# Kernel optimization log

Measured on AMD Instinct MI355X. Metric: run time of the kernel, lower is better.

Reference implementation:

```python
import jax, jax.numpy as jnp
import numpy as np

D = 128      # dim_emb
FF = 512     # dim_ff
H = 8        # nb_heads
HD = D // H
NLE = 2      # encoder layers (action and state)
NLD = 2      # decoder layers
NS = 1       # num_state_encoder
TANH_CLIP = 10.0
BIG = jnp.float32(1e9)


def layer_norm(h, g, b):
    mu = jnp.mean(h, -1, keepdims=True)
    v = jnp.var(h, -1, keepdims=True)
    return g * (h - mu) * jax.lax.rsqrt(v + 1e-5) + b


def mha_self(h, Wq, Wk, Wv, Wo, bq, bk, bv, bo):
    B, S, _ = h.shape
    q = (h @ Wq + bq).reshape(B, S, H, HD)
    k = (h @ Wk + bk).reshape(B, S, H, HD)
    v = (h @ Wv + bv).reshape(B, S, H, HD)
    a = jax.nn.softmax(jnp.einsum('bqhd,bkhd->bhqk', q, k) / np.float32(np.sqrt(HD)), axis=-1)
    return jnp.einsum('bhqk,bkhd->bqhd', a, v).reshape(B, S, D) @ Wo + bo


def encode(tok, Wemb, bemb, aW, aB, W1, b1, W2, b2, ln):
    # tok: [B, S, 2] raw coordinates -> [B, S, D]
    h = tok @ Wemb + bemb
    for l in range(NLE):
        h = layer_norm(h + mha_self(h, *aW[l], *aB[l]), ln[l, 0, 0], ln[l, 0, 1])
        ffo = jax.nn.relu(h @ W1[l] + b1[l]) @ W2[l] + b2[l]
        h = layer_norm(h + ffo, ln[l, 1, 0], ln[l, 1, 1])
    return h


def _forward(x, start_idx, action_k, state_k,
             a_emb_W, a_emb_b, a_attn_W, a_attn_b, a_ff_W1, a_ff_b1, a_ff_W2, a_ff_b2, a_ln,
             s_emb_W, s_emb_b, s_attn_W, s_attn_b, s_ff_W1, s_ff_b1, s_ff_W2, s_ff_b2, s_ln,
             WK, bK, WV, bV, Wq_mlp, bq_mlp, d_Wq, d_bq, d_Wo, d_bo):
    B, N, _ = x.shape
    bar = jnp.arange(B)
    first = x[bar, start_idx]                                   # [B,2]
    mask0 = jnp.ones((B, N), bool).at[bar, start_idx].set(False)  # True = unvisited
    ka, ks = action_k, state_k

    def step(carry, _):
        mask, last_idx, logp = carry
        last = x[bar, last_idx]                                  # [B,2]
        # knn over unvisited nodes (visited nodes pushed to distance BIG)
        d2 = jnp.sum((x - last[:, None, :]) ** 2, -1)
        d2 = jnp.where(mask, d2, BIG)
        _, knn_idx = jax.lax.top_k(-d2, ks)                      # [B,ks] nearest-first global node ids
        aidx = knn_idx[:, :ka]                                   # [B,ka]
        valid = mask[bar[:, None], aidx]                         # unvisited -> valid action
        # action encoder: k_action neighbors + last visited node
        tok_a = jnp.concatenate([x[bar[:, None], aidx], last[:, None, :]], 1)       # [B,ka+1,2]
        emb_a = encode(tok_a, a_emb_W, a_emb_b, a_attn_W, a_attn_b, a_ff_W1, a_ff_b1, a_ff_W2, a_ff_b2, a_ln)
        emb_q = emb_a[:, ka]
        emb_o = emb_a[:, :ka]
        # state encoder: k_state neighbors + last + first visited node
        tok_s = jnp.concatenate([x[bar[:, None], knn_idx], last[:, None, :], first[:, None, :]], 1)  # [B,ks+2,2]
        emb_s = encode(tok_s, s_emb_W, s_emb_b, s_attn_W, s_attn_b, s_ff_W1, s_ff_b1, s_ff_W2, s_ff_b2, s_ln)
        emb_q = jnp.concatenate([emb_q, emb_s[:, ks], emb_s[:, ks + 1]], -1)        # [B,(2*NS+1)*D]
        emb_o = jnp.concatenate([emb_o, emb_s[:, :ka]], -1)                          # [B,ka,(NS+1)*D]
        # decoder: per-layer K/V slices, masked cross-attention, final tanh-clipped pointer
        h = emb_q @ Wq_mlp + bq_mlp                              # [B,D]
        K = (emb_o @ WK + bK).reshape(B, ka, NLD, D)
        V = (emb_o @ WV + bV).reshape(B, ka, NLD, D)
        for l in range(NLD - 1):
            q = (h @ d_Wq[l] + d_bq[l]).reshape(B, H, HD)
            kk = K[:, :, l].reshape(B, ka, H, HD)
            vv = V[:, :, l].reshape(B, ka, H, HD)
            sc = jnp.einsum('bhd,bkhd->bhk', q, kk) / np.float32(np.sqrt(HD))
            sc = jnp.where(valid[:, None, :], sc, -BIG)
            o = jnp.einsum('bhk,bkhd->bhd', jax.nn.softmax(sc, -1), vv).reshape(B, D) @ d_Wo[l] + d_bo[l]
            h = h + o
        q = h @ d_Wq[NLD - 1] + d_bq[NLD - 1]
        logits = TANH_CLIP * jnp.tanh(jnp.einsum('bd,bkd->bk', q, K[:, :, NLD - 1]) / np.float32(np.sqrt(D)))
        logits = jnp.where(valid, logits, -BIG)
        prob = jax.nn.softmax(logits, -1)
        idx = jnp.argmax(prob, 1)                                # deterministic choice
        nxt = aidx[bar, idx]
        logp = logp + jnp.log(prob[bar, idx])
        mask = mask.at[bar, nxt].set(False)
        return (mask, nxt, logp), nxt

    (_, _, logp), ys = jax.lax.scan(step, (mask0, start_idx, jnp.zeros(B, jnp.float32)), None, length=N - 1)
    tours = jnp.concatenate([start_idx[:, None], ys.T], 1)       # [B,N]
    return tours, logp


def setup_inputs() -> dict:
    key = jax.random.key(0)
    ks = jax.random.split(key, 16)
    def Nrm(k, shape, fan):
        return jax.random.normal(k, shape, jnp.float32) / np.float32(np.sqrt(fan))
    B, Nn = 64, 50
    inp = {}
    inp['x'] = jax.random.uniform(ks[0], (B, Nn, 2), jnp.float32)
    inp['start_idx'] = jax.random.randint(ks[1], (B,), 0, Nn)
    inp['action_k'] = 15
    inp['state_k'] = 35
    inp['a_emb_W'] = Nrm(ks[2], (2, D), 2); inp['a_emb_b'] = jnp.zeros((D,))
    inp['a_attn_W'] = Nrm(ks[3], (NLE, 4, D, D), D); inp['a_attn_b'] = jnp.zeros((NLE, 4, D))
    inp['a_ff_W1'] = Nrm(ks[4], (NLE, D, FF), D); inp['a_ff_b1'] = jnp.zeros((NLE, FF))
    inp['a_ff_W2'] = Nrm(ks[5], (NLE, FF, D), FF); inp['a_ff_b2'] = jnp.zeros((NLE, D))
    inp['a_ln'] = jnp.stack([jnp.ones((NLE, 2, D)), jnp.zeros((NLE, 2, D))], 2)
    inp['s_emb_W'] = Nrm(ks[6], (2, D), 2); inp['s_emb_b'] = jnp.zeros((D,))
    inp['s_attn_W'] = Nrm(ks[7], (NLE, 4, D, D), D); inp['s_attn_b'] = jnp.zeros((NLE, 4, D))
    inp['s_ff_W1'] = Nrm(ks[8], (NLE, D, FF), D); inp['s_ff_b1'] = jnp.zeros((NLE, FF))
    inp['s_ff_W2'] = Nrm(ks[9], (NLE, FF, D), FF); inp['s_ff_b2'] = jnp.zeros((NLE, D))
    inp['s_ln'] = jnp.stack([jnp.ones((NLE, 2, D)), jnp.zeros((NLE, 2, D))], 2)
    inp['WK'] = Nrm(ks[10], ((NS + 1) * D, NLD * D), (NS + 1) * D); inp['bK'] = jnp.zeros((NLD * D,))
    inp['WV'] = Nrm(ks[11], ((NS + 1) * D, NLD * D), (NS + 1) * D); inp['bV'] = jnp.zeros((NLD * D,))
    inp['Wq_mlp'] = Nrm(ks[12], ((2 * NS + 1) * D, D), (2 * NS + 1) * D); inp['bq_mlp'] = jnp.zeros((D,))
    inp['d_Wq'] = Nrm(ks[13], (NLD, D, D), D); inp['d_bq'] = jnp.zeros((NLD, D))
    inp['d_Wo'] = Nrm(ks[14], (NLD, D, D), D); inp['d_bo'] = jnp.zeros((NLD, D))
    return inp


def reference(x, start_idx, action_k, state_k,
              a_emb_W, a_emb_b, a_attn_W, a_attn_b, a_ff_W1, a_ff_b1, a_ff_W2, a_ff_b2, a_ln,
              s_emb_W, s_emb_b, s_attn_W, s_attn_b, s_ff_W1, s_ff_b1, s_ff_W2, s_ff_b2, s_ln,
              WK, bK, WV, bV, Wq_mlp, bq_mlp, d_Wq, d_bq, d_Wo, d_bo):
    return _forward(x, start_idx, action_k, state_k,
                    a_emb_W, a_emb_b, a_attn_W, a_attn_b, a_ff_W1, a_ff_b1, a_ff_W2, a_ff_b2, a_ln,
                    s_emb_W, s_emb_b, s_attn_W, s_attn_b, s_ff_W1, s_ff_b1, s_ff_W2, s_ff_b2, s_ln,
                    WK, bK, WV, bV, Wq_mlp, bq_mlp, d_Wq, d_bq, d_Wo, d_bo)
```

## Files before the change

kernel.cpp:

```cpp
#include <hip/hip_runtime.h>
#include <hip/hip_bf16.h>

namespace {

constexpr int NB  = 64;
constexpr int NN  = 50;
constexpr int DM  = 128;
constexpr int FFDIM = 512;
constexpr int NHD = 8;
constexpr int HDM = 16;
constexpr int KA  = 15;
constexpr int KS  = 35;
constexpr int TA  = 16;
constexpr int TS  = 37;
constexpr int NT  = 512;
constexpr float BIGF = 1000000000.0f;

constexpr int OFF_H    = 0;
constexpr int OFF_EMBA = TS * DM;
constexpr int OFF_SCR  = OFF_EMBA + TA * DM;
constexpr int SCR_FLOATS = 3 * TS * DM + NHD * TS * TS;
constexpr int SMEM_FLOATS = OFF_SCR + SCR_FLOATS;
constexpr int SMEM_BYTES  = SMEM_FLOATS * 4;

struct Params {
  const float* x; const int* start;
  const float* a_emb_W; const float* a_emb_b;
  const float* a_attn_W; const float* a_attn_b;
  const float* a_ff_W1; const float* a_ff_b1;
  const float* a_ff_W2; const float* a_ff_b2;
  const float* a_ln;
  const float* s_emb_W; const float* s_emb_b;
  const float* s_attn_W; const float* s_attn_b;
  const float* s_ff_W1; const float* s_ff_b1;
  const float* s_ff_W2; const float* s_ff_b2;
  const float* s_ln;
  const float* WK; const float* bK;
  const float* WV; const float* bV;
  const float* Wq_mlp; const float* bq_mlp;
  const float* d_Wq; const float* d_bq;
  const float* d_Wo; const float* d_bo;
  float* out;
};

template<int R>
__device__ inline void matmul_rt(const float* __restrict__ in, int lda,
                                 const float* __restrict__ W, int ldw,
                                 const float* __restrict__ bias,
                                 float* __restrict__ out, int ldo,
                                 int T, int K, int C, bool relu, int tid)
{
  const int c4 = C >> 2;
  const int cw = tid & (c4 - 1);
  const int g  = tid / c4;
  const int ng = NT / c4;
  const int c  = cw << 2;
  const float4 bv = *(const float4*)(bias + c);
#define FMA16_(aa, i) \
  acc[i].x = fmaf((aa).x, w0.x, acc[i].x); acc[i].y = fmaf((aa).x, w0.y, acc[i].y); \
  acc[i].z = fmaf((aa).x, w0.z, acc[i].z); acc[i].w = fmaf((aa).x, w0.w, acc[i].w); \
  acc[i].x = fmaf((aa).y, w1.x, acc[i].x); acc[i].y = fmaf((aa).y, w1.y, acc[i].y); \
  acc[i].z = fmaf((aa).y, w1.z, acc[i].z); acc[i].w = fmaf((aa).y, w1.w, acc[i].w); \
  acc[i].x = fmaf((aa).z, w2.x, acc[i].x); acc[i].y = fmaf((aa).z, w2.y, acc[i].y); \
  acc[i].z = fmaf((aa).z, w2.z, acc[i].z); acc[i].w = fmaf((aa).z, w2.w, acc[i].w); \
  acc[i].x = fmaf((aa).w, w3.x, acc[i].x); acc[i].y = fmaf((aa).w, w3.y, acc[i].y); \
  acc[i].z = fmaf((aa).w, w3.z, acc[i].z); acc[i].w = fmaf((aa).w, w3.w, acc[i].w);
  for (int rb = g * R; rb < T; rb += ng * R) {
    float4 acc[R];
#pragma unroll
    for (int i = 0; i < R; ++i) acc[i] = bv;
    const float* __restrict__ wp = W + c;
    const float* __restrict__ ip = in + rb * lda;
#pragma unroll 2
    for (int kk = 0; kk < K; kk += 4) {
      float4 w0 = *(const float4*)(wp + (size_t)(kk    ) * ldw);
      float4 w1 = *(const float4*)(wp + (size_t)(kk + 1) * ldw);
      float4 w2 = *(const float4*)(wp + (size_t)(kk + 2) * ldw);
      float4 w3 = *(const float4*)(wp + (size_t)(kk + 3) * ldw);
#pragma unroll
      for (int i = 0; i < R; ++i) {
        float4 a = *(const float4*)(ip + i * lda + kk);
        FMA16_(a, i);
      }
    }
#pragma unroll
    for (int i = 0; i < R; ++i) {
      if (rb + i < T) {
        float4 r2 = acc[i];
        if (relu) {
          r2.x = fmaxf(r2.x, 0.f); r2.y = fmaxf(r2.y, 0.f);
          r2.z = fmaxf(r2.z, 0.f); r2.w = fmaxf(r2.w, 0.f);
        }
        *(float4*)(out + (rb + i) * ldo + c) = r2;
      }
    }
  }
#undef FMA16_
}

__device__ inline void matvec128(const float* __restrict__ in, const float* __restrict__ W,
                                 const float* __restrict__ bias, float* __restrict__ out,
                                 int K, float* __restrict__ red, int tid)
{
  const int c = tid & 127;
  const int s = tid >> 7;
  const int ks = K >> 2;
  const int k0 = s * ks;
  float acc = 0.f;
#pragma unroll 8
  for (int k = k0; k < k0 + ks; ++k) acc = fmaf(in[k], W[(size_t)k * 128 + c], acc);
  red[tid] = acc;
  __syncthreads();
  if (tid < 128) out[c] = bias[c] + ((red[c] + red[128 + c]) + (red[256 + c] + red[384 + c]));
  __syncthreads();
}

__device__ inline void layernorm_add(float* __restrict__ h, const float* __restrict__ add,
                                     const float* __restrict__ g, const float* __restrict__ bta,
                                     int T, int tid)
{
  const int lane = tid & 63;
  const int wv = tid >> 6;
  for (int r = wv; r < T; r += NT / 64) {
    float v0 = h[r * DM + lane]      + add[r * DM + lane];
    float v1 = h[r * DM + lane + 64] + add[r * DM + lane + 64];
    float sum = v0 + v1;
    for (int off = 32; off; off >>= 1) sum += __shfl_xor(sum, off);
    float mu = sum * (1.0f / 128.0f);
    float d0 = v0 - mu, d1 = v1 - mu;
    float sq = d0 * d0 + d1 * d1;
    for (int off = 32; off; off >>= 1) sq += __shfl_xor(sq, off);
    float rs = 1.0f / sqrtf(sq * (1.0f / 128.0f) + 1e-5f);
    h[r * DM + lane]      = g[lane]      * d0 * rs + bta[lane];
    h[r * DM + lane + 64] = g[lane + 64] * d1 * rs + bta[lane + 64];
  }
}

template<int T, int RQK, int RFF>
__device__ void encode_block(float* __restrict__ h, float* __restrict__ scr,
                             const float* __restrict__ tok,
                             const float* __restrict__ embW, const float* __restrict__ embB,
                             const float* __restrict__ attnW, const float* __restrict__ attnB,
                             const float* __restrict__ W1, const float* __restrict__ b1,
                             const float* __restrict__ W2, const float* __restrict__ b2,
                             const float* __restrict__ ln, int tid)
{
  const int lane = tid & 63;
  const int wv = tid >> 6;
  for (int idx = tid; idx < T * DM; idx += NT) {
    int r = idx >> 7, c = idx & (DM - 1);
    h[idx] = tok[2 * r] * embW[c] + tok[2 * r + 1] * embW[DM + c] + embB[c];
  }
  __syncthreads();
  float* q = scr;
  float* k = scr + TS * DM;
  float* v = scr + 2 * TS * DM;
  float* s = scr + 3 * TS * DM;
  for (int l = 0; l < 2; ++l) {
    const float* Wq = attnW + (size_t)(l * 4 + 0) * DM * DM;
    const float* Wk = attnW + (size_t)(l * 4 + 1) * DM * DM;
    const float* Wv = attnW + (size_t)(l * 4 + 2) * DM * DM;
    const float* Wo = attnW + (size_t)(l * 4 + 3) * DM * DM;
    const float* bq = attnB + (l * 4 + 0) * DM;
    const float* bk = attnB + (l * 4 + 1) * DM;
    const float* bv = attnB + (l * 4 + 2) * DM;
    const float* bo = attnB + (l * 4 + 3) * DM;
    matmul_rt<RQK>(h, DM, Wq, DM, bq, q, DM, T, DM, DM, false, tid);
    matmul_rt<RQK>(h, DM, Wk, DM, bk, k, DM, T, DM, DM, false, tid);
    matmul_rt<RQK>(h, DM, Wv, DM, bv, v, DM, T, DM, DM, false, tid);
    __syncthreads();
    constexpr int TT = T * T;
    for (int idx = tid; idx < NHD * TT; idx += NT) {
      int hd = idx / TT; int rem = idx - hd * TT; int i = rem / T; int j = rem - i * T;
      const float4* q4 = (const float4*)(q + i * DM + hd * HDM);
      const float4* k4 = (const float4*)(k + j * DM + hd * HDM);
      float acc = 0.f;
#pragma unroll
      for (int d = 0; d < 4; ++d) {
        float4 qa = q4[d], ka = k4[d];
        acc += qa.x * ka.x + qa.y * ka.y + qa.z * ka.z + qa.w * ka.w;
      }
      s[(hd * T + i) * T + j] = acc * 0.25f;
    }
    __syncthreads();
    for (int r = wv; r < NHD * T; r += NT / 64) {
      float val = (lane < T) ? s[r * T + lane] : -INFINITY;
      float mx = val;
      for (int off = 32; off; off >>= 1) mx = fmaxf(mx, __shfl_xor(mx, off));
      float e = (lane < T) ? expf(val - mx) : 0.f;
      float sum = e;
      for (int off = 32; off; off >>= 1) sum += __shfl_xor(sum, off);
      if (lane < T) s[r * T + lane] = e / sum;
    }
    __syncthreads();
    for (int idx = tid; idx < T * DM; idx += NT) {
      int i = idx >> 7, c = idx & (DM - 1); int hd = c >> 4;
      const float* ar = s + (hd * T + i) * T;
      float acc = 0.f;
#pragma unroll 4
      for (int j = 0; j < T; ++j) acc = fmaf(ar[j], v[j * DM + c], acc);
      q[idx] = acc;
    }
    __syncthreads();
    matmul_rt<RQK>(q, DM, Wo, DM, bo, k, DM, T, DM, DM, false, tid);
    __syncthreads();
    layernorm_add(h, k, ln + ((l * 2 + 0) * 2 + 0) * DM, ln + ((l * 2 + 0) * 2 + 1) * DM, T, tid);
    __syncthreads();
    const float* W1l = W1 + (size_t)l * DM * FFDIM;
    const float* b1l = b1 + l * FFDIM;
    matmul_rt<RFF>(h, DM, W1l, FFDIM, b1l, scr, FFDIM, T, DM, 256, true, tid);
    matmul_rt<RFF>(h, DM, W1l + 256, FFDIM, b1l + 256, scr + 256, FFDIM, T, DM, 256, true, tid);
    __syncthreads();
    matmul_rt<RQK>(scr, FFDIM, W2 + (size_t)l * FFDIM * DM, DM, b2 + l * DM,
                   scr + TS * FFDIM, DM, T, FFDIM, DM, false, tid);
    __syncthreads();
    layernorm_add(h, scr + TS * FFDIM, ln + ((l * 2 + 1) * 2 + 0) * DM, ln + ((l * 2 + 1) * 2 + 1) * DM, T, tid);
    __syncthreads();
  }
}

__global__ __launch_bounds__(NT, 1)
void tsp_kernel(Params p)
{
  const int b = blockIdx.x;
  const int tid = threadIdx.x;
  const int lane = tid & 63;
  const int wv = tid >> 6;

  extern __shared__ float sm[];
  float* sh   = sm + OFF_H;
  float* emba = sm + OFF_EMBA;
  float* scr  = sm + OFF_SCR;

  __shared__ float xl[NN * 2];
  __shared__ int   maskS[NN];
  __shared__ int   knnS[KS];
  __shared__ int   validS[KA];
  __shared__ float d2S[NN];
  __shared__ float tokA[TA * 2];
  __shared__ float tokS[TS * 2];
  __shared__ int   lastS;
  __shared__ float logpS;

  for (int i = tid; i < NN * 2; i += NT) xl[i] = p.x[b * NN * 2 + i];
  const int st = p.start[b];
  for (int i = tid; i < NN; i += NT) maskS[i] = (i != st) ? 1 : 0;
  if (tid == 0) {
    lastS = st; logpS = 0.f;
    p.out[b * NN] = (float)st;
  }
  __syncthreads();
  const float fx = xl[2 * st], fy = xl[2 * st + 1];

  for (int t = 0; t < NN - 1; ++t) {
    const int last = lastS;
    const float lx = xl[2 * last], ly = xl[2 * last + 1];

    for (int j = tid; j < NN; j += NT) {
      float dx = __fsub_rn(xl[2 * j], lx);
      float dy = __fsub_rn(xl[2 * j + 1], ly);
      float dd = __fadd_rn(__fmul_rn(dx, dx), __fmul_rn(dy, dy));
      d2S[j] = maskS[j] ? dd : BIGF;
    }
    __syncthreads();

    if (wv == 0) {
      float v = (lane < NN) ? d2S[lane] : 2.0f * BIGF;
      const int vi = lane;
      for (int s2 = 0; s2 < KS; ++s2) {
        float mv = v; int mi = vi;
        for (int off = 32; off; off >>= 1) {
          float ov = __shfl_xor(mv, off);
          int oi = __shfl_xor(mi, off);
          if (ov < mv || (ov == mv && oi < mi)) { mv = ov; mi = oi; }
        }
        if (lane == 0) knnS[s2] = mi;
        if (vi == mi) v = 4.0f * BIGF;
      }
    }
    __syncthreads();

    if (tid < KA) validS[tid] = maskS[knnS[tid]];
    if (tid < KS) { int j = knnS[tid]; tokS[2 * tid] = xl[2 * j]; tokS[2 * tid + 1] = xl[2 * j + 1]; }
    if (tid < KA) { int j = knnS[tid]; tokA[2 * tid] = xl[2 * j]; tokA[2 * tid + 1] = xl[2 * j + 1]; }
    if (tid == NT - 1) { tokA[2 * KA] = lx; tokA[2 * KA + 1] = ly; }
    if (tid == NT - 2) { tokS[2 * KS] = lx; tokS[2 * KS + 1] = ly; }
    if (tid == NT - 3) { tokS[2 * KS + 2] = fx; tokS[2 * KS + 3] = fy; }
    __syncthreads();

    encode_block<TA, 1, 2>(sh, scr, tokA, p.a_emb_W, p.a_emb_b, p.a_attn_W, p.a_attn_b,
                           p.a_ff_W1, p.a_ff_b1, p.a_ff_W2, p.a_ff_b2, p.a_ln, tid);
    for (int i = tid; i < TA * DM; i += NT) emba[i] = sh[i];
    __syncthreads();

    encode_block<TS, 3, 5>(sh, scr, tokS, p.s_emb_W, p.s_emb_b, p.s_attn_W, p.s_attn_b,
                           p.s_ff_W1, p.s_ff_b1, p.s_ff_W2, p.s_ff_b2, p.s_ln, tid);

    float* embq = scr;
    float* embo = scr + 384;
    float* Kd   = scr + 4224;
    float* Vd   = scr + 8064;
    float* hdec = scr + 11904;
    float* qd   = scr + 12032;
    float* scd  = scr + 12160;
    float* od   = scr + 12288;
    float* tmp  = scr + 12416;
    float* red  = scr + 12544;

    if (tid < 384) {
      embq[tid] = (tid < 128) ? emba[KA * DM + tid]
                : (tid < 256) ? sh[KS * DM + (tid - 128)]
                              : sh[(KS + 1) * DM + (tid - 256)];
    }
    for (int idx = tid; idx < KA * 256; idx += NT) {
      int r = idx >> 8, c = idx & 255;
      embo[idx] = (c < 128) ? emba[r * DM + c] : sh[r * DM + (c - 128)];
    }
    __syncthreads();

    matmul_rt<2>(embo, 256, p.WK, 256, p.bK, Kd, 256, KA, 256, 256, false, tid);
    matmul_rt<2>(embo, 256, p.WV, 256, p.bV, Vd, 256, KA, 256, 256, false, tid);
    matvec128(embq, p.Wq_mlp, p.bq_mlp, hdec, 384, red, tid);

    matvec128(hdec, p.d_Wq, p.d_bq, qd, DM, red, tid);
    if (tid < NHD * KA) {
      int hd = tid / KA, kk2 = tid - hd * KA;
      const float* qh = qd + hd * HDM;
      const float* kh = Kd + kk2 * 256 + hd * HDM;
      float acc = 0.f;
#pragma unroll
      for (int d = 0; d < HDM; ++d) acc += qh[d] * kh[d];
      acc = acc / 4.0f;
      scd[tid] = validS[kk2] ? acc : -BIGF;
    }
    __syncthreads();
    if (tid < NHD) {
      float mx = -INFINITY;
#pragma unroll
      for (int kk2 = 0; kk2 < KA; ++kk2) mx = fmaxf(mx, scd[tid * KA + kk2]);
      float e[KA]; float sum = 0.f;
#pragma unroll
      for (int kk2 = 0; kk2 < KA; ++kk2) { e[kk2] = expf(scd[tid * KA + kk2] - mx); sum += e[kk2]; }
      float inv = 1.0f / sum;
#pragma unroll
      for (int kk2 = 0; kk2 < KA; ++kk2) scd[tid * KA + kk2] = e[kk2] * inv;
    }
    __syncthreads();
    if (tid < DM) {
      int hd = tid >> 4;
      float acc = 0.f;
#pragma unroll
      for (int kk2 = 0; kk2 < KA; ++kk2) acc = fmaf(scd[hd * KA + kk2], Vd[kk2 * 256 + tid], acc);
      od[tid] = acc;
    }
    __syncthreads();
    matvec128(od, p.d_Wo, p.d_bo, tmp, DM, red, tid);
    if (tid < DM) hdec[tid] += tmp[tid];
    __syncthreads();

    matvec128(hdec, p.d_Wq + DM * DM, p.d_bq + DM, qd, DM, red, tid);
    if (wv == 0) {
      float lg = -BIGF;
      if (lane < KA) {
        const float* kf = Kd + lane * 256 + 128;
        float acc = 0.f;
#pragma unroll 8
        for (int d = 0; d < DM; ++d) acc = fmaf(qd[d], kf[d], acc);
        acc = acc / 11.313708498984761f;
        lg = validS[lane] ? 10.0f * tanhf(acc) : -BIGF;
      }
      float mv = lg; int mi = (lane < KA) ? lane : 1000;
      for (int off = 32; off; off >>= 1) {
        float ov = __shfl_xor(mv, off);
        int oi = __shfl_xor(mi, off);
        if (ov > mv || (ov == mv && oi < mi)) { mv = ov; mi = oi; }
      }
      float e = (lane < KA) ? expf(lg - mv) : 0.f;
      float sum = e;
      for (int off = 32; off; off >>= 1) sum += __shfl_xor(sum, off);
      if (lane == 0) {
        int nxt = knnS[mi];
        logpS += -logf(sum);
        maskS[nxt] = 0;
        lastS = nxt;
        p.out[b * NN + t + 1] = (float)nxt;
      }
    }
    __syncthreads();
  }

  if (tid == 0) p.out[NB * NN + b] = logpS;
}

}

extern "C" void kernel_launch(void* const* d_in, const int* in_sizes, int n_in,
                              void* d_out, int out_size, void* d_ws, size_t ws_size,
                              hipStream_t stream)
{
  (void)in_sizes; (void)n_in; (void)out_size; (void)d_ws; (void)ws_size;
  Params p;
  p.x        = (const float*)d_in[0];
  p.start    = (const int*)d_in[1];
  p.a_emb_W  = (const float*)d_in[4];
  p.a_emb_b  = (const float*)d_in[5];
  p.a_attn_W = (const float*)d_in[6];
  p.a_attn_b = (const float*)d_in[7];
  p.a_ff_W1  = (const float*)d_in[8];
  p.a_ff_b1  = (const float*)d_in[9];
  p.a_ff_W2  = (const float*)d_in[10];
  p.a_ff_b2  = (const float*)d_in[11];
  p.a_ln     = (const float*)d_in[12];
  p.s_emb_W  = (const float*)d_in[13];
  p.s_emb_b  = (const float*)d_in[14];
  p.s_attn_W = (const float*)d_in[15];
  p.s_attn_b = (const float*)d_in[16];
  p.s_ff_W1  = (const float*)d_in[17];
  p.s_ff_b1  = (const float*)d_in[18];
  p.s_ff_W2  = (const float*)d_in[19];
  p.s_ff_b2  = (const float*)d_in[20];
  p.s_ln     = (const float*)d_in[21];
  p.WK       = (const float*)d_in[22];
  p.bK       = (const float*)d_in[23];
  p.WV       = (const float*)d_in[24];
  p.bV       = (const float*)d_in[25];
  p.Wq_mlp   = (const float*)d_in[26];
  p.bq_mlp   = (const float*)d_in[27];
  p.d_Wq     = (const float*)d_in[28];
  p.d_bq     = (const float*)d_in[29];
  p.d_Wo     = (const float*)d_in[30];
  p.d_bo     = (const float*)d_in[31];
  p.out      = (float*)d_out;

  (void)hipFuncSetAttribute((const void*)tsp_kernel,
                            hipFuncAttributeMaxDynamicSharedMemorySize, SMEM_BYTES);
  tsp_kernel<<<NB, NT, SMEM_BYTES, stream>>>(p);
}
```

Measured before the change: 42.29 ms.

## Run action and state encoders concurrently on split thread groups of a 1024-thread block

Doubles the block to 1024 threads and splits it into a 256-thread group that encodes the action tokens and a 768-thread group that encodes the state tokens at the same time, each with its own shared-memory region. This removes the serial back-to-back encoder passes and the copy of the action embeddings. Attention is chunked over heads and the feed-forward over hidden halves, with accumulation into the output, so the larger shared-memory split fits. The catch is that __syncthreads inside encode_block now covers both groups, which have different loop trip counts; this could deadlock or force the shorter group to wait, and fewer waves per SIMD may fit because of the larger block.

```diff
diff --git a/kernel.cpp b/kernel.cpp
--- a/kernel.cpp
+++ b/kernel.cpp
@@ -1,5 +1,4 @@
 #include <hip/hip_runtime.h>
-#include <hip/hip_bf16.h>
 
 namespace {
 
@@ -13,14 +12,14 @@
 constexpr int KS  = 35;
 constexpr int TA  = 16;
 constexpr int TS  = 37;
-constexpr int NT  = 512;
+constexpr int NT  = 1024;
 constexpr float BIGF = 1000000000.0f;
 
-constexpr int OFF_H    = 0;
-constexpr int OFF_EMBA = TS * DM;
-constexpr int OFF_SCR  = OFF_EMBA + TA * DM;
-constexpr int SCR_FLOATS = 3 * TS * DM + NHD * TS * TS;
-constexpr int SMEM_FLOATS = OFF_SCR + SCR_FLOATS;
+constexpr int OFF_HA   = 0;
+constexpr int OFF_SCRA = 2048;
+constexpr int OFF_HS   = 9216;
+constexpr int OFF_SCRS = 13952;
+constexpr int SMEM_FLOATS = 33664;
 constexpr int SMEM_BYTES  = SMEM_FLOATS * 4;
 
 struct Params {
@@ -43,19 +42,19 @@
   float* out;
 };
 
-template<int R>
+template<int R, int C, int K>
 __device__ inline void matmul_rt(const float* __restrict__ in, int lda,
                                  const float* __restrict__ W, int ldw,
                                  const float* __restrict__ bias,
                                  float* __restrict__ out, int ldo,
-                                 int T, int K, int C, bool relu, int tid)
-{
-  const int c4 = C >> 2;
+                                 int T, bool relu, bool accum,
+                                 int tid, int nth)
+{
+  constexpr int c4 = C >> 2;
   const int cw = tid & (c4 - 1);
   const int g  = tid / c4;
-  const int ng = NT / c4;
+  const int ng = nth / c4;
   const int c  = cw << 2;
-  const float4 bv = *(const float4*)(bias + c);
 #define FMA16_(aa, i) \
   acc[i].x = fmaf((aa).x, w0.x, acc[i].x); acc[i].y = fmaf((aa).x, w0.y, acc[i].y); \
   acc[i].z = fmaf((aa).x, w0.z, acc[i].z); acc[i].w = fmaf((aa).x, w0.w, acc[i].w); \
@@ -67,8 +66,14 @@
   acc[i].z = fmaf((aa).w, w3.z, acc[i].z); acc[i].w = fmaf((aa).w, w3.w, acc[i].w);
   for (int rb = g * R; rb < T; rb += ng * R) {
     float4 acc[R];
-#pragma unroll
-    for (int i = 0; i < R; ++i) acc[i] = bv;
+    if (accum) {
+#pragma unroll
+      for (int i = 0; i < R; ++i) acc[i] = *(const float4*)(out + (rb + i) * ldo + c);
+    } else {
+      const float4 bv = *(const float4*)(bias + c);
+#pragma unroll
+      for (int i = 0; i < R; ++i) acc[i] = bv;
+    }
     const float* __restrict__ wp = W + c;
     const float* __restrict__ ip = in + rb * lda;
 #pragma unroll 2
@@ -104,24 +109,29 @@
 {
   const int c = tid & 127;
   const int s = tid >> 7;
-  const int ks = K >> 2;
+  const int ks = K >> 3;
   const int k0 = s * ks;
   float acc = 0.f;
 #pragma unroll 8
   for (int k = k0; k < k0 + ks; ++k) acc = fmaf(in[k], W[(size_t)k * 128 + c], acc);
   red[tid] = acc;
   __syncthreads();
-  if (tid < 128) out[c] = bias[c] + ((red[c] + red[128 + c]) + (red[256 + c] + red[384 + c]));
+  if (tid < 128) {
+    float sum = ((red[c] + red[128 + c]) + (red[256 + c] + red[384 + c]))
+              + ((red[512 + c] + red[640 + c]) + (red[768 + c] + red[896 + c]));
+    out[c] = bias[c] + sum;
+  }
   __syncthreads();
 }
 
 __device__ inline void layernorm_add(float* __restrict__ h, const float* __restrict__ add,
                                      const float* __restrict__ g, const float* __restrict__ bta,
-                                     int T, int tid)
+                                     int T, int tid, int nth)
 {
   const int lane = tid & 63;
-  const int wv = tid >> 6;
-  for (int r = wv; r < T; r += NT / 64) {
+  const int wvl = tid >> 6;
+  const int nwv = nth >> 6;
+  for (int r = wvl; r < T; r += nwv) {
     float v0 = h[r * DM + lane]      + add[r * DM + lane];
     float v1 = h[r * DM + lane + 64] + add[r * DM + lane + 64];
     float sum = v0 + v1;
@@ -136,26 +146,27 @@
   }
 }
 
-template<int T, int RQK, int RFF>
 __device__ void encode_block(float* __restrict__ h, float* __restrict__ scr,
-                             const float* __restrict__ tok,
+                             const float* __restrict__ tok, int T,
                              const float* __restrict__ embW, const float* __restrict__ embB,
                              const float* __restrict__ attnW, const float* __restrict__ attnB,
                              const float* __restrict__ W1, const float* __restrict__ b1,
                              const float* __restrict__ W2, const float* __restrict__ b2,
-                             const float* __restrict__ ln, int tid)
+                             const float* __restrict__ ln, int tid, int nth)
 {
   const int lane = tid & 63;
-  const int wv = tid >> 6;
-  for (int idx = tid; idx < T * DM; idx += NT) {
-    int r = idx >> 7, c = idx & (DM - 1);
+  const int wvl = tid >> 6;
+  const int nwv = nth >> 6;
+  for (int idx = tid; idx < T * DM; idx += nth) {
+    int r = idx >> 7, c = idx & 127;
     h[idx] = tok[2 * r] * embW[c] + tok[2 * r + 1] * embW[DM + c] + embB[c];
   }
   __syncthreads();
   float* q = scr;
-  float* k = scr + TS * DM;
-  float* v = scr + 2 * TS * DM;
-  float* s = scr + 3 * TS * DM;
+  float* k = scr + T * DM;
+  float* v = scr + 2 * T * DM;
+  float* s = scr + 3 * T * DM;
+  const int TT = T * T;
   for (int l = 0; l < 2; ++l) {
     const float* Wq = attnW + (size_t)(l * 4 + 0) * DM * DM;
     const float* Wk = attnW + (size_t)(l * 4 + 1) * DM * DM;
@@ -165,61 +176,67 @@
     const float* bk = attnB + (l * 4 + 1) * DM;
     const float* bv = attnB + (l * 4 + 2) * DM;
     const float* bo = attnB + (l * 4 + 3) * DM;
-    matmul_rt<RQK>(h, DM, Wq, DM, bq, q, DM, T, DM, DM, false, tid);
-    matmul_rt<RQK>(h, DM, Wk, DM, bk, k, DM, T, DM, DM, false, tid);
-    matmul_rt<RQK>(h, DM, Wv, DM, bv, v, DM, T, DM, DM, false, tid);
-    __syncthreads();
-    constexpr int TT = T * T;
-    for (int idx = tid; idx < NHD * TT; idx += NT) {
-      int hd = idx / TT; int rem = idx - hd * TT; int i = rem / T; int j = rem - i * T;
-      const float4* q4 = (const float4*)(q + i * DM + hd * HDM);
-      const float4* k4 = (const float4*)(k + j * DM + hd * HDM);
-      float acc = 0.f;
-#pragma unroll
-      for (int d = 0; d < 4; ++d) {
-        float4 qa = q4[d], ka = k4[d];
-        acc += qa.x * ka.x + qa.y * ka.y + qa.z * ka.z + qa.w * ka.w;
-      }
-      s[(hd * T + i) * T + j] = acc * 0.25f;
-    }
-    __syncthreads();
-    for (int r = wv; r < NHD * T; r += NT / 64) {
-      float val = (lane < T) ? s[r * T + lane] : -INFINITY;
-      float mx = val;
-      for (int off = 32; off; off >>= 1) mx = fmaxf(mx, __shfl_xor(mx, off));
-      float e = (lane < T) ? expf(val - mx) : 0.f;
-      float sum = e;
-      for (int off = 32; off; off >>= 1) sum += __shfl_xor(sum, off);
-      if (lane < T) s[r * T + lane] = e / sum;
-    }
-    __syncthreads();
-    for (int idx = tid; idx < T * DM; idx += NT) {
-      int i = idx >> 7, c = idx & (DM - 1); int hd = c >> 4;
-      const float* ar = s + (hd * T + i) * T;
-      float acc = 0.f;
+    matmul_rt<2,128,128>(h, DM, Wq, DM, bq, q, DM, T, false, false, tid, nth);
+    matmul_rt<2,128,128>(h, DM, Wk, DM, bk, k, DM, T, false, false, tid, nth);
+    matmul_rt<2,128,128>(h, DM, Wv, DM, bv, v, DM, T, false, false, tid, nth);
+    __syncthreads();
+    for (int ch = 0; ch < 2; ++ch) {
+      for (int idx = tid; idx < 4 * TT; idx += nth) {
+        int hd4 = idx / TT; int rem = idx - hd4 * TT; int i = rem / T; int j = rem - i * T;
+        int hd = ch * 4 + hd4;
+        const float4* q4 = (const float4*)(q + i * DM + hd * HDM);
+        const float4* k4 = (const float4*)(k + j * DM + hd * HDM);
+        float acc = 0.f;
+#pragma unroll
+        for (int d = 0; d < 4; ++d) {
+          float4 qa = q4[d], ka = k4[d];
+          acc += qa.x * ka.x + qa.y * ka.y + qa.z * ka.z + qa.w * ka.w;
+        }
+        s[idx] = acc * 0.25f;
+      }
+      __syncthreads();
+      for (int r = wvl; r < 4 * T; r += nwv) {
+        float val = (lane < T) ? s[r * T + lane] : -INFINITY;
+        float mx = val;
+        for (int off = 32; off; off >>= 1) mx = fmaxf(mx, __shfl_xor(mx, off));
+        float e = (lane < T) ? expf(val - mx) : 0.f;
+        float sum = e;
+        for (int off = 32; off; off >>= 1) sum += __shfl_xor(sum, off);
+        if (lane < T) s[r * T + lane] = e / sum;
+      }
+      __syncthreads();
+      for (int idx = tid; idx < T * 64; idx += nth) {
+        int i = idx >> 6; int cc = idx & 63; int col = ch * 64 + cc; int hd4 = cc >> 4;
+        const float* ar = s + (hd4 * T + i) * T;
+        float acc = 0.f;
 #pragma unroll 4
-      for (int j = 0; j < T; ++j) acc = fmaf(ar[j], v[j * DM + c], acc);
-      q[idx] = acc;
-    }
-    __syncthreads();
-    matmul_rt<RQK>(q, DM, Wo, DM, bo, k, DM, T, DM, DM, false, tid);
-    __syncthreads();
-    layernorm_add(h, k, ln + ((l * 2 + 0) * 2 + 0) * DM, ln + ((l * 2 + 0) * 2 + 1) * DM, T, tid);
+        for (int j = 0; j < T; ++j) acc = fmaf(ar[j], v[j * DM + col], acc);
+        q[i * DM + col] = acc;
+      }
+      __syncthreads();
+    }
+    matmul_rt<2,128,128>(q, DM, Wo, DM, bo, k, DM, T, false, false, tid, nth);
+    __syncthreads();
+    layernorm_add(h, k, ln + ((l * 2 + 0) * 2 + 0) * DM, ln + ((l * 2 + 0) * 2 + 1) * DM, T, tid, nth);
     __syncthreads();
     const float* W1l = W1 + (size_t)l * DM * FFDIM;
     const float* b1l = b1 + l * FFDIM;
-    matmul_rt<RFF>(h, DM, W1l, FFDIM, b1l, scr, FFDIM, T, DM, 256, true, tid);
-    matmul_rt<RFF>(h, DM, W1l + 256, FFDIM, b1l + 256, scr + 256, FFDIM, T, DM, 256, true, tid);
-    __syncthreads();
-    matmul_rt<RQK>(scr, FFDIM, W2 + (size_t)l * FFDIM * DM, DM, b2 + l * DM,
-                   scr + TS * FFDIM, DM, T, FFDIM, DM, false, tid);
-    __syncthreads();
-    layernorm_add(h, scr + TS * FFDIM, ln + ((l * 2 + 1) * 2 + 0) * DM, ln + ((l * 2 + 1) * 2 + 1) * DM, T, tid);
-    __syncthreads();
-  }
-}
-
-__global__ __launch_bounds__(NT, 1)
+    const float* W2l = W2 + (size_t)l * FFDIM * DM;
+    float* hidden = scr;
+    float* ff2out = scr + T * 256;
+    for (int ch = 0; ch < 2; ++ch) {
+      matmul_rt<4,256,128>(h, DM, W1l + ch * 256, FFDIM, b1l + ch * 256, hidden, 256, T, true, false, tid, nth);
+      __syncthreads();
+      matmul_rt<2,128,256>(hidden, 256, W2l + (size_t)ch * 256 * DM, DM, b2 + l * DM,
+                           ff2out, DM, T, false, (ch == 1), tid, nth);
+      __syncthreads();
+    }
+    layernorm_add(h, ff2out, ln + ((l * 2 + 1) * 2 + 0) * DM, ln + ((l * 2 + 1) * 2 + 1) * DM, T, tid, nth);
+    __syncthreads();
+  }
+}
+
+__global__ __launch_bounds__(NT)
 void tsp_kernel(Params p)
 {
   const int b = blockIdx.x;
@@ -228,9 +245,10 @@
   const int wv = tid >> 6;
 
   extern __shared__ float sm[];
-  float* sh   = sm + OFF_H;
-  float* emba = sm + OFF_EMBA;
-  float* scr  = sm + OFF_SCR;
+  float* hA   = sm + OFF_HA;
+  float* scrA = sm + OFF_SCRA;
+  float* hS   = sm + OFF_HS;
+  float* scrS = sm + OFF_SCRS;
 
   __shared__ float xl[NN * 2];
   __shared__ int   maskS[NN];
@@ -241,6 +259,23 @@
   __shared__ float tokS[TS * 2];
   __shared__ int   lastS;
   __shared__ float logpS;
+
+  const int half = (tid >= 256) ? 1 : 0;
+  const int tl   = half ? tid - 256 : tid;
+  const int nth  = half ? 768 : 256;
+  float* hX   = half ? hS : hA;
+  float* scrX = half ? scrS : scrA;
+  const float* tokX = half ? tokS : tokA;
+  const int TX = half ? TS : TA;
+  const float* eW  = half ? p.s_emb_W  : p.a_emb_W;
+  const float* eB  = half ? p.s_emb_b  : p.a_emb_b;
+  const float* aW  = half ? p.s_attn_W : p.a_attn_W;
+  const float* aB  = half ? p.s_attn_b : p.a_attn_b;
+  const float* fW1 = half ? p.s_ff_W1  : p.a_ff_W1;
+  const float* fb1 = half ? p.s_ff_b1  : p.a_ff_b1;
+  const float* fW2 = half ? p.s_ff_W2  : p.a_ff_W2;
+  const float* fb2 = half ? p.s_ff_b2  : p.a_ff_b2;
+  const float* lnX = half ? p.s_ln     : p.a_ln;
 
   for (int i = tid; i < NN * 2; i += NT) xl[i] = p.x[b * NN * 2 + i];
   const int st = p.start[b];
@@ -288,38 +323,32 @@
     if (tid == NT - 3) { tokS[2 * KS + 2] = fx; tokS[2 * KS + 3] = fy; }
     __syncthreads();
 
-    encode_block<TA, 1, 2>(sh, scr, tokA, p.a_emb_W, p.a_emb_b, p.a_attn_W, p.a_attn_b,
-                           p.a_ff_W1, p.a_ff_b1, p.a_ff_W2, p.a_ff_b2, p.a_ln, tid);
-    for (int i = tid; i < TA * DM; i += NT) emba[i] = sh[i];
-    __syncthreads();
-
-    encode_block<TS, 3, 5>(sh, scr, tokS, p.s_emb_W, p.s_emb_b, p.s_attn_W, p.s_attn_b,
-                           p.s_ff_W1, p.s_ff_b1, p.s_ff_W2, p.s_ff_b2, p.s_ln, tid);
-
-    float* embq = scr;
-    float* embo = scr + 384;
-    float* Kd   = scr + 4224;
-    float* Vd   = scr + 8064;
-    float* hdec = scr + 11904;
-    float* qd   = scr + 12032;
-    float* scd  = scr + 12160;
-    float* od   = scr + 12288;
-    float* tmp  = scr + 12416;
-    float* red  = scr + 12544;
+    encode_block(hX, scrX, tokX, TX, eW, eB, aW, aB, fW1, fb1, fW2, fb2, lnX, tl, nth);
+
+    float* embq = scrS;
+    float* embo = scrS + 384;
+    float* Kd   = scrS + 4224;
+    float* Vd   = scrS + 8064;
+    float* hdec = scrS + 11904;
+    float* qd   = scrS + 12032;
+    float* scd  = scrS + 12160;
+    float* od   = scrS + 12288;
+    float* tmp  = scrS + 12416;
+    float* red  = scrS + 12544;
 
     if (tid < 384) {
-      embq[tid] = (tid < 128) ? emba[KA * DM + tid]
-                : (tid < 256) ? sh[KS * DM + (tid - 128)]
-                              : sh[(KS + 1) * DM + (tid - 256)];
+      embq[tid] = (tid < 128) ? hA[KA * DM + tid]
+                : (tid < 256) ? hS[KS * DM + (tid - 128)]
+                              : hS[(KS + 1) * DM + (tid - 256)];
     }
     for (int idx = tid; idx < KA * 256; idx += NT) {
       int r = idx >> 8, c = idx & 255;
-      embo[idx] = (c < 128) ? emba[r * DM + c] : sh[r * DM + (c - 128)];
-    }
-    __syncthreads();
-
-    matmul_rt<2>(embo, 256, p.WK, 256, p.bK, Kd, 256, KA, 256, 256, false, tid);
-    matmul_rt<2>(embo, 256, p.WV, 256, p.bV, Vd, 256, KA, 256, 256, false, tid);
+      embo[idx] = (c < 128) ? hA[r * DM + c] : hS[r * DM + (c - 128)];
+    }
+    __syncthreads();
+
+    matmul_rt<1,256,256>(embo, 256, p.WK, 256, p.bK, Kd, 256, KA, false, false, tid, NT);
+    matmul_rt<1,256,256>(embo, 256, p.WV, 256, p.bV, Vd, 256, KA, false, false, tid, NT);
     matvec128(embq, p.Wq_mlp, p.bq_mlp, hdec, 384, red, tid);
 
     matvec128(hdec, p.d_Wq, p.d_bq, qd, DM, red, tid);
```

New measurement: 41.79 ms. About the same (-1.2%).

## Double block threads and fuse QKV and FF matmuls into multi-matrix launches

Applied to the files above, without the earlier changes.

Raises the block size from 512 to 1024 threads and replaces the row-tiled matmul with a block-assigned version. In it, groups of threads compute several weight matrices (Q, K, V, or the four FF1 column blocks) in one pass, with software-prefetched weight loads. FF2 is split along K across two thread groups and reduced inside the layernorm. Separate buffers for the action and state encodings remove a copy, and the matvec reduction now sums 8 partials. The goal is more parallelism per step at the cost of register pressure and occupancy limits from 1024-thread blocks.

```diff
diff --git a/kernel.cpp b/kernel.cpp
--- a/kernel.cpp
+++ b/kernel.cpp
@@ -1,5 +1,4 @@
 #include <hip/hip_runtime.h>
-#include <hip/hip_bf16.h>
 
 namespace {
 
@@ -13,13 +12,13 @@
 constexpr int KS  = 35;
 constexpr int TA  = 16;
 constexpr int TS  = 37;
-constexpr int NT  = 512;
+constexpr int NT  = 1024;
 constexpr float BIGF = 1000000000.0f;
 
-constexpr int OFF_H    = 0;
-constexpr int OFF_EMBA = TS * DM;
-constexpr int OFF_SCR  = OFF_EMBA + TA * DM;
-constexpr int SCR_FLOATS = 3 * TS * DM + NHD * TS * TS;
+constexpr int OFF_HA  = 0;
+constexpr int OFF_HS  = 2048;
+constexpr int OFF_SCR = 6784;
+constexpr int SCR_FLOATS = 28416;
 constexpr int SMEM_FLOATS = OFF_SCR + SCR_FLOATS;
 constexpr int SMEM_BYTES  = SMEM_FLOATS * 4;
 
@@ -44,58 +43,83 @@
 };
 
 template<int R>
-__device__ inline void matmul_rt(const float* __restrict__ in, int lda,
-                                 const float* __restrict__ W, int ldw,
-                                 const float* __restrict__ bias,
-                                 float* __restrict__ out, int ldo,
-                                 int T, int K, int C, bool relu, int tid)
-{
-  const int c4 = C >> 2;
-  const int cw = tid & (c4 - 1);
-  const int g  = tid / c4;
-  const int ng = NT / c4;
-  const int c  = cw << 2;
-  const float4 bv = *(const float4*)(bias + c);
-#define FMA16_(aa, i) \
-  acc[i].x = fmaf((aa).x, w0.x, acc[i].x); acc[i].y = fmaf((aa).x, w0.y, acc[i].y); \
-  acc[i].z = fmaf((aa).x, w0.z, acc[i].z); acc[i].w = fmaf((aa).x, w0.w, acc[i].w); \
-  acc[i].x = fmaf((aa).y, w1.x, acc[i].x); acc[i].y = fmaf((aa).y, w1.y, acc[i].y); \
-  acc[i].z = fmaf((aa).y, w1.z, acc[i].z); acc[i].w = fmaf((aa).y, w1.w, acc[i].w); \
-  acc[i].x = fmaf((aa).z, w2.x, acc[i].x); acc[i].y = fmaf((aa).z, w2.y, acc[i].y); \
-  acc[i].z = fmaf((aa).z, w2.z, acc[i].z); acc[i].w = fmaf((aa).z, w2.w, acc[i].w); \
-  acc[i].x = fmaf((aa).w, w3.x, acc[i].x); acc[i].y = fmaf((aa).w, w3.y, acc[i].y); \
-  acc[i].z = fmaf((aa).w, w3.z, acc[i].z); acc[i].w = fmaf((aa).w, w3.w, acc[i].w);
-  for (int rb = g * R; rb < T; rb += ng * R) {
-    float4 acc[R];
-#pragma unroll
-    for (int i = 0; i < R; ++i) acc[i] = bv;
-    const float* __restrict__ wp = W + c;
-    const float* __restrict__ ip = in + rb * lda;
-#pragma unroll 2
-    for (int kk = 0; kk < K; kk += 4) {
-      float4 w0 = *(const float4*)(wp + (size_t)(kk    ) * ldw);
-      float4 w1 = *(const float4*)(wp + (size_t)(kk + 1) * ldw);
-      float4 w2 = *(const float4*)(wp + (size_t)(kk + 2) * ldw);
-      float4 w3 = *(const float4*)(wp + (size_t)(kk + 3) * ldw);
-#pragma unroll
-      for (int i = 0; i < R; ++i) {
-        float4 a = *(const float4*)(ip + i * lda + kk);
-        FMA16_(a, i);
-      }
-    }
-#pragma unroll
-    for (int i = 0; i < R; ++i) {
-      if (rb + i < T) {
-        float4 r2 = acc[i];
-        if (relu) {
-          r2.x = fmaxf(r2.x, 0.f); r2.y = fmaxf(r2.y, 0.f);
-          r2.z = fmaxf(r2.z, 0.f); r2.w = fmaxf(r2.w, 0.f);
-        }
-        *(float4*)(out + (rb + i) * ldo + c) = r2;
-      }
-    }
-  }
-#undef FMA16_
+__device__ inline void fma4(float4* acc, const float* __restrict__ in, const int* ro, int kb,
+                            float4 w0, float4 w1, float4 w2, float4 w3)
+{
+#pragma unroll
+  for (int i = 0; i < R; ++i) {
+    float4 a = *(const float4*)(in + ro[i] + kb);
+    acc[i].x = fmaf(a.x,w0.x,acc[i].x); acc[i].y = fmaf(a.x,w0.y,acc[i].y);
+    acc[i].z = fmaf(a.x,w0.z,acc[i].z); acc[i].w = fmaf(a.x,w0.w,acc[i].w);
+    acc[i].x = fmaf(a.y,w1.x,acc[i].x); acc[i].y = fmaf(a.y,w1.y,acc[i].y);
+    acc[i].z = fmaf(a.y,w1.z,acc[i].z); acc[i].w = fmaf(a.y,w1.w,acc[i].w);
+    acc[i].x = fmaf(a.z,w2.x,acc[i].x); acc[i].y = fmaf(a.z,w2.y,acc[i].y);
+    acc[i].z = fmaf(a.z,w2.z,acc[i].z); acc[i].w = fmaf(a.z,w2.w,acc[i].w);
+    acc[i].x = fmaf(a.w,w3.x,acc[i].x); acc[i].y = fmaf(a.w,w3.y,acc[i].y);
+    acc[i].z = fmaf(a.w,w3.z,acc[i].z); acc[i].w = fmaf(a.w,w3.w,acc[i].w);
+  }
+}
+
+template<int R, int NG, int NM, int K>
+__device__ inline void matmul_blk(const float* __restrict__ in, int lda,
+                                  const float* __restrict__ W, int ldw, int wBlk,
+                                  const float* __restrict__ bias,
+                                  float* __restrict__ out, int ldo, int outBlk,
+                                  int T, bool relu, int tid, int tid0)
+{
+  constexpr int NACT = NG * NM * 32;
+  const int t = tid - tid0;
+  if (t < 0 || t >= NACT) return;
+  const int cw = t % (NM * 32);
+  const int g  = t / (NM * 32);
+  const int m  = cw >> 5;
+  const int c  = (cw & 31) << 2;
+  const float* __restrict__ wp = W + (size_t)m * wBlk + c;
+  float* __restrict__ op = out + (size_t)m * outBlk + c;
+  const int rb = g * R;
+  int ro[R];
+#pragma unroll
+  for (int i = 0; i < R; ++i) ro[i] = min(rb + i, T - 1) * lda;
+  float4 acc[R];
+  if (bias) {
+    const float4 bv4 = *(const float4*)(bias + m * 128 + c);
+#pragma unroll
+    for (int i = 0; i < R; ++i) acc[i] = bv4;
+  } else {
+#pragma unroll
+    for (int i = 0; i < R; ++i) acc[i] = make_float4(0.f, 0.f, 0.f, 0.f);
+  }
+  float4 wA0, wA1, wA2, wA3, wB0, wB1, wB2, wB3;
+  wA0 = *(const float4*)(wp + (size_t)0 * ldw);
+  wA1 = *(const float4*)(wp + (size_t)1 * ldw);
+  wA2 = *(const float4*)(wp + (size_t)2 * ldw);
+  wA3 = *(const float4*)(wp + (size_t)3 * ldw);
+#pragma unroll 1
+  for (int kk = 0; kk < K; kk += 8) {
+    wB0 = *(const float4*)(wp + (size_t)(kk + 4) * ldw);
+    wB1 = *(const float4*)(wp + (size_t)(kk + 5) * ldw);
+    wB2 = *(const float4*)(wp + (size_t)(kk + 6) * ldw);
+    wB3 = *(const float4*)(wp + (size_t)(kk + 7) * ldw);
+    fma4<R>(acc, in, ro, kk, wA0, wA1, wA2, wA3);
+    if (kk + 8 < K) {
+      wA0 = *(const float4*)(wp + (size_t)(kk +  8) * ldw);
+      wA1 = *(const float4*)(wp + (size_t)(kk +  9) * ldw);
+      wA2 = *(const float4*)(wp + (size_t)(kk + 10) * ldw);
+      wA3 = *(const float4*)(wp + (size_t)(kk + 11) * ldw);
+    }
+    fma4<R>(acc, in, ro, kk + 4, wB0, wB1, wB2, wB3);
+  }
+#pragma unroll
+  for (int i = 0; i < R; ++i) {
+    if (rb + i < T) {
+      float4 r2 = acc[i];
+      if (relu) {
+        r2.x = fmaxf(r2.x, 0.f); r2.y = fmaxf(r2.y, 0.f);
+        r2.z = fmaxf(r2.z, 0.f); r2.w = fmaxf(r2.w, 0.f);
+      }
+      *(float4*)(op + (rb + i) * ldo) = r2;
+    }
+  }
 }
 
 __device__ inline void matvec128(const float* __restrict__ in, const float* __restrict__ W,
@@ -104,26 +128,32 @@
 {
   const int c = tid & 127;
   const int s = tid >> 7;
-  const int ks = K >> 2;
+  const int ks = K >> 3;
   const int k0 = s * ks;
   float acc = 0.f;
 #pragma unroll 8
   for (int k = k0; k < k0 + ks; ++k) acc = fmaf(in[k], W[(size_t)k * 128 + c], acc);
   red[tid] = acc;
   __syncthreads();
-  if (tid < 128) out[c] = bias[c] + ((red[c] + red[128 + c]) + (red[256 + c] + red[384 + c]));
+  if (tid < 128) {
+    float sum = ((red[c] + red[128 + c]) + (red[256 + c] + red[384 + c]))
+              + ((red[512 + c] + red[640 + c]) + (red[768 + c] + red[896 + c]));
+    out[c] = bias[c] + sum;
+  }
   __syncthreads();
 }
 
-__device__ inline void layernorm_add(float* __restrict__ h, const float* __restrict__ add,
-                                     const float* __restrict__ g, const float* __restrict__ bta,
-                                     int T, int tid)
+__device__ inline void layernorm_add2(float* __restrict__ h, const float* __restrict__ a1,
+                                      const float* __restrict__ a2,
+                                      const float* __restrict__ g, const float* __restrict__ bta,
+                                      int T, int tid)
 {
   const int lane = tid & 63;
-  const int wv = tid >> 6;
-  for (int r = wv; r < T; r += NT / 64) {
-    float v0 = h[r * DM + lane]      + add[r * DM + lane];
-    float v1 = h[r * DM + lane + 64] + add[r * DM + lane + 64];
+  const int wvl = tid >> 6;
+  for (int r = wvl; r < T; r += NT / 64) {
+    float v0 = h[r * DM + lane]      + a1[r * DM + lane];
+    float v1 = h[r * DM + lane + 64] + a1[r * DM + lane + 64];
+    if (a2) { v0 += a2[r * DM + lane]; v1 += a2[r * DM + lane + 64]; }
     float sum = v0 + v1;
     for (int off = 32; off; off >>= 1) sum += __shfl_xor(sum, off);
     float mu = sum * (1.0f / 128.0f);
@@ -136,7 +166,7 @@
   }
 }
 
-template<int T, int RQK, int RFF>
+template<int T, int R, int NG>
 __device__ void encode_block(float* __restrict__ h, float* __restrict__ scr,
                              const float* __restrict__ tok,
                              const float* __restrict__ embW, const float* __restrict__ embB,
@@ -146,30 +176,22 @@
                              const float* __restrict__ ln, int tid)
 {
   const int lane = tid & 63;
-  const int wv = tid >> 6;
+  const int wvl = tid >> 6;
+  constexpr int TT = T * T;
+  float* q = scr;
+  float* k = scr + T * DM;
+  float* v = scr + 2 * T * DM;
+  float* s = scr + 3 * T * DM;
   for (int idx = tid; idx < T * DM; idx += NT) {
-    int r = idx >> 7, c = idx & (DM - 1);
+    int r = idx >> 7, c = idx & 127;
     h[idx] = tok[2 * r] * embW[c] + tok[2 * r + 1] * embW[DM + c] + embB[c];
   }
   __syncthreads();
-  float* q = scr;
-  float* k = scr + TS * DM;
-  float* v = scr + 2 * TS * DM;
-  float* s = scr + 3 * TS * DM;
   for (int l = 0; l < 2; ++l) {
-    const float* Wq = attnW + (size_t)(l * 4 + 0) * DM * DM;
-    const float* Wk = attnW + (size_t)(l * 4 + 1) * DM * DM;
-    const float* Wv = attnW + (size_t)(l * 4 + 2) * DM * DM;
-    const float* Wo = attnW + (size_t)(l * 4 + 3) * DM * DM;
-    const float* bq = attnB + (l * 4 + 0) * DM;
-    const float* bk = attnB + (l * 4 + 1) * DM;
-    const float* bv = attnB + (l * 4 + 2) * DM;
-    const float* bo = attnB + (l * 4 + 3) * DM;
-    matmul_rt<RQK>(h, DM, Wq, DM, bq, q, DM, T, DM, DM, false, tid);
-    matmul_rt<RQK>(h, DM, Wk, DM, bk, k, DM, T, DM, DM, false, tid);
-    matmul_rt<RQK>(h, DM, Wv, DM, bv, v, DM, T, DM, DM, false, tid);
-    __syncthreads();
-    constexpr int TT = T * T;
+    const float* Wq = attnW + (size_t)(l * 4) * DM * DM;
+    const float* bq = attnB + (l * 4) * DM;
+    matmul_blk<R, NG, 3, DM>(h, DM, Wq, DM, DM * DM, bq, q, DM, T * DM, T, false, tid, 0);
+    __syncthreads();
     for (int idx = tid; idx < NHD * TT; idx += NT) {
       int hd = idx / TT; int rem = idx - hd * TT; int i = rem / T; int j = rem - i * T;
       const float4* q4 = (const float4*)(q + i * DM + hd * HDM);
@@ -180,10 +202,10 @@
         float4 qa = q4[d], ka = k4[d];
         acc += qa.x * ka.x + qa.y * ka.y + qa.z * ka.z + qa.w * ka.w;
       }
-      s[(hd * T + i) * T + j] = acc * 0.25f;
-    }
-    __syncthreads();
-    for (int r = wv; r < NHD * T; r += NT / 64) {
+      s[idx] = acc * 0.25f;
+    }
+    __syncthreads();
+    for (int r = wvl; r < NHD * T; r += NT / 64) {
       float val = (lane < T) ? s[r * T + lane] : -INFINITY;
       float mx = val;
       for (int off = 32; off; off >>= 1) mx = fmaxf(mx, __shfl_xor(mx, off));
@@ -194,7 +216,7 @@
     }
     __syncthreads();
     for (int idx = tid; idx < T * DM; idx += NT) {
-      int i = idx >> 7, c = idx & (DM - 1); int hd = c >> 4;
+      int i = idx >> 7, c = idx & 127; int hd = c >> 4;
       const float* ar = s + (hd * T + i) * T;
       float acc = 0.f;
 #pragma unroll 4
@@ -202,24 +224,30 @@
       q[idx] = acc;
     }
     __syncthreads();
-    matmul_rt<RQK>(q, DM, Wo, DM, bo, k, DM, T, DM, DM, false, tid);
-    __syncthreads();
-    layernorm_add(h, k, ln + ((l * 2 + 0) * 2 + 0) * DM, ln + ((l * 2 + 0) * 2 + 1) * DM, T, tid);
+    matmul_blk<R, NG, 1, DM>(q, DM, Wq + (size_t)3 * DM * DM, DM, 0, bq + 3 * DM,
+                             v, DM, 0, T, false, tid, 0);
+    __syncthreads();
+    layernorm_add2(h, v, nullptr, ln + ((l * 2 + 0) * 2 + 0) * DM, ln + ((l * 2 + 0) * 2 + 1) * DM, T, tid);
     __syncthreads();
     const float* W1l = W1 + (size_t)l * DM * FFDIM;
     const float* b1l = b1 + l * FFDIM;
-    matmul_rt<RFF>(h, DM, W1l, FFDIM, b1l, scr, FFDIM, T, DM, 256, true, tid);
-    matmul_rt<RFF>(h, DM, W1l + 256, FFDIM, b1l + 256, scr + 256, FFDIM, T, DM, 256, true, tid);
-    __syncthreads();
-    matmul_rt<RQK>(scr, FFDIM, W2 + (size_t)l * FFDIM * DM, DM, b2 + l * DM,
-                   scr + TS * FFDIM, DM, T, FFDIM, DM, false, tid);
-    __syncthreads();
-    layernorm_add(h, scr + TS * FFDIM, ln + ((l * 2 + 1) * 2 + 0) * DM, ln + ((l * 2 + 1) * 2 + 1) * DM, T, tid);
-    __syncthreads();
-  }
-}
-
-__global__ __launch_bounds__(NT, 1)
+    const float* W2l = W2 + (size_t)l * FFDIM * DM;
+    float* hidden = scr;
+    float* ff2o   = scr + T * FFDIM;
+    float* ff2b   = ff2o + T * DM;
+    matmul_blk<R, NG, 4, DM>(h, DM, W1l, FFDIM, 128, b1l, hidden, FFDIM, 128, T, true, tid, 0);
+    __syncthreads();
+    matmul_blk<R, NG, 1, 256>(hidden, FFDIM, W2l, DM, 0, b2 + l * DM,
+                              ff2o, DM, 0, T, false, tid, 0);
+    matmul_blk<R, NG, 1, 256>(hidden + 256, FFDIM, W2l + (size_t)256 * DM, DM, 0, nullptr,
+                              ff2b, DM, 0, T, false, tid, 256);
+    __syncthreads();
+    layernorm_add2(h, ff2o, ff2b, ln + ((l * 2 + 1) * 2 + 0) * DM, ln + ((l * 2 + 1) * 2 + 1) * DM, T, tid);
+    __syncthreads();
+  }
+}
+
+__global__ __launch_bounds__(NT)
 void tsp_kernel(Params p)
 {
   const int b = blockIdx.x;
@@ -228,9 +256,9 @@
   const int wv = tid >> 6;
 
   extern __shared__ float sm[];
-  float* sh   = sm + OFF_H;
-  float* emba = sm + OFF_EMBA;
-  float* scr  = sm + OFF_SCR;
+  float* hA  = sm + OFF_HA;
+  float* hS  = sm + OFF_HS;
+  float* scr = sm + OFF_SCR;
 
   __shared__ float xl[NN * 2];
   __shared__ int   maskS[NN];
@@ -288,12 +316,9 @@
     if (tid == NT - 3) { tokS[2 * KS + 2] = fx; tokS[2 * KS + 3] = fy; }
     __syncthreads();
 
-    encode_block<TA, 1, 2>(sh, scr, tokA, p.a_emb_W, p.a_emb_b, p.a_attn_W, p.a_attn_b,
+    encode_block<TA, 4, 4>(hA, scr, tokA, p.a_emb_W, p.a_emb_b, p.a_attn_W, p.a_attn_b,
                            p.a_ff_W1, p.a_ff_b1, p.a_ff_W2, p.a_ff_b2, p.a_ln, tid);
-    for (int i = tid; i < TA * DM; i += NT) emba[i] = sh[i];
-    __syncthreads();
-
-    encode_block<TS, 3, 5>(sh, scr, tokS, p.s_emb_W, p.s_emb_b, p.s_attn_W, p.s_attn_b,
+    encode_block<TS, 8, 5>(hS, scr, tokS, p.s_emb_W, p.s_emb_b, p.s_attn_W, p.s_attn_b,
                            p.s_ff_W1, p.s_ff_b1, p.s_ff_W2, p.s_ff_b2, p.s_ln, tid);
 
     float* embq = scr;
@@ -308,18 +333,18 @@
     float* red  = scr + 12544;
 
     if (tid < 384) {
-      embq[tid] = (tid < 128) ? emba[KA * DM + tid]
-                : (tid < 256) ? sh[KS * DM + (tid - 128)]
-                              : sh[(KS + 1) * DM + (tid - 256)];
+      embq[tid] = (tid < 128) ? hA[KA * DM + tid]
+                : (tid < 256) ? hS[KS * DM + (tid - 128)]
+                              : hS[(KS + 1) * DM + (tid - 256)];
     }
     for (int idx = tid; idx < KA * 256; idx += NT) {
       int r = idx >> 8, c = idx & 255;
-      embo[idx] = (c < 128) ? emba[r * DM + c] : sh[r * DM + (c - 128)];
-    }
-    __syncthreads();
-
-    matmul_rt<2>(embo, 256, p.WK, 256, p.bK, Kd, 256, KA, 256, 256, false, tid);
-    matmul_rt<2>(embo, 256, p.WV, 256, p.bV, Vd, 256, KA, 256, 256, false, tid);
+      embo[idx] = (c < 128) ? hA[r * DM + c] : hS[r * DM + (c - 128)];
+    }
+    __syncthreads();
+
+    matmul_blk<8, 2, 2, 256>(embo, 256, p.WK, 256, 128, p.bK, Kd, 256, 128, KA, false, tid, 0);
+    matmul_blk<8, 2, 2, 256>(embo, 256, p.WV, 256, 128, p.bV, Vd, 256, 128, KA, false, tid, 128);
     matvec128(embq, p.Wq_mlp, p.bq_mlp, hdec, 384, red, tid);
 
     matvec128(hdec, p.d_Wq, p.d_bq, qd, DM, red, tid);
```

New measurement: 43.83 ms. 1.04x slower.
